# Optimization experiments

Measured on AMD Instinct MI355X. Metric: run time of the kernel, lower is better.

## Reference

```python
import jax, jax.numpy as jnp
import numpy as np

B, L, D_MODEL, H, DK = 4, 1024, 1024, 16, 64
FILTER_LENGTHS = (2, 4)
FMAX = max(FILTER_LENGTHS)


def setup_inputs() -> dict:
    key = jax.random.key(0)
    ks = jax.random.split(key, 12)
    s = 0.02
    inp = {
        "Q": jax.random.normal(ks[0], (B, L, D_MODEL), jnp.float32),
        "K": jax.random.normal(ks[1], (B, L, D_MODEL), jnp.float32),
        "V": jax.random.normal(ks[2], (B, L, D_MODEL), jnp.float32),
        "attn_mask": jnp.zeros((1,), jnp.bool_),
        "WQ": jax.random.normal(ks[3], (D_MODEL, H * DK), jnp.float32) * s,
        "bQ": jnp.zeros((H * DK,), jnp.float32),
        "WK": jax.random.normal(ks[4], (D_MODEL, H * DK), jnp.float32) * s,
        "bK": jnp.zeros((H * DK,), jnp.float32),
        "WV": jax.random.normal(ks[5], (D_MODEL, H * DK), jnp.float32) * s,
        "bV": jnp.zeros((H * DK,), jnp.float32),
        "Wfc": jax.random.normal(ks[6], (H * DK, D_MODEL), jnp.float32) * s,
        "bfc": jnp.zeros((D_MODEL,), jnp.float32),
        "conv_q": jax.random.normal(ks[7], (H * DK, H * DK, FMAX), jnp.float32) * s,
        "conv_k": jax.random.normal(ks[8], (H * DK, H * DK, FMAX), jnp.float32) * s,
        "w": jax.random.normal(ks[9], (len(FILTER_LENGTHS),), jnp.float32),
    }
    return inp


def _get_conv(x4, conv, w):
    # x4: (b, h, l, d_k) -> ACAT.get_conv with torch-identical raw reshapes
    b, h, l, d_k = x4.shape
    sig = x4.reshape(b, h * d_k, l)            # raw row-major reshape (as torch)
    pad = jnp.pad(sig, ((0, 0), (0, 0), (FMAX // 2, FMAX // 2)))
    idx = jnp.arange(l)[:, None] + jnp.arange(FMAX)[None, :]   # (l, FMAX) unfold windows
    seq = pad[:, :, idx]                        # (b, d, l, FMAX)
    f_s = jnp.array(FILTER_LENGTHS, dtype=sig.dtype)
    w_f = f_s * w                               # einsum('f,f->f')
    ind = jnp.argmax(w_f)
    flen = jnp.array(FILTER_LENGTHS)[ind]
    mask = (jnp.arange(FMAX) < flen).astype(sig.dtype)
    seq = seq * mask                            # zero out trailing taps
    out = jnp.einsum('bdlf,dof->blo', seq, conv)  # o = h*d_k
    return out.reshape(b, h, l, d_k)            # raw reshape as in torch code


def reference(Q, K, V, attn_mask, WQ, bQ, WK, bK, WV, bV, Wfc, bfc, conv_q, conv_k, w):
    b, l, _ = Q.shape
    q = (Q @ WQ + bQ).reshape(b, l, H, DK).transpose(0, 2, 1, 3)  # (b,h,l,dk)
    k = (K @ WK + bK).reshape(b, l, H, DK).transpose(0, 2, 1, 3)
    v = (V @ WV + bV).reshape(b, l, H, DK).transpose(0, 2, 1, 3)
    q = _get_conv(q, conv_q, w) + q
    k = _get_conv(k, conv_k, w) + k
    scores = jnp.einsum('bhqd,bhkd->bhqk', q, k) / np.sqrt(DK).astype(np.float32)
    attn = jax.nn.softmax(scores, axis=-1)
    ctx = jnp.einsum('bhqk,bhkd->bhqd', attn, v)
    ctx = ctx.transpose(0, 2, 1, 3).reshape(b, l, H * DK)
    out = ctx @ Wfc + bfc
    return out
```

## Files before the change

### kernel.cpp

```cpp
#include <hip/hip_runtime.h>
#include <hip/hip_bf16.h>

typedef _Float16 f16;
typedef _Float16 f16x2 __attribute__((ext_vector_type(2)));
typedef _Float16 f16x4 __attribute__((ext_vector_type(4)));
typedef _Float16 f16x8 __attribute__((ext_vector_type(8)));
typedef float f32x4 __attribute__((ext_vector_type(4)));

__device__ __forceinline__ f16x2 pkrtz(float a, float b) {
    auto r = __builtin_amdgcn_cvt_pkrtz(a, b);
    f16x2 o; o[0] = (f16)r[0]; o[1] = (f16)r[1];
    return o;
}

#define XT_ROWS 1027
#define XT_BSTRIDE (XT_ROWS * 1024)

__device__ __forceinline__ void gload16(const f16* g, f16* l) {
    __builtin_amdgcn_global_load_lds(
        (const __attribute__((address_space(1))) void*)g,
        (__attribute__((address_space(3))) void*)l, 16, 0, 0);
}

__device__ __forceinline__ void stage_tile(const f16* src, int ld, f16* lds)
{
    const int tid = threadIdx.x;
    const int w512 = (tid >> 6) << 9;
    #pragma unroll
    for (int q = 0; q < 4; ++q) {
        const int s = q * 256 + tid;
        const int row = s >> 3;
        const int col = ((s & 7) ^ (row & 7)) << 3;
        gload16(src + row * ld + col, lds + (q << 11) + w512);
    }
}

__device__ __forceinline__ void stage64(const f16* src, int ld, f16* lds)
{
    const int tid = threadIdx.x;
    const int w512 = (tid >> 6) << 9;
    #pragma unroll
    for (int q = 0; q < 2; ++q) {
        const int s = q * 256 + tid;
        const int row = s >> 3;
        const int col = ((s & 7) ^ (row & 7)) << 3;
        gload16(src + row * ld + col, lds + (q << 11) + w512);
    }
}

template <int CONV>
__device__ __forceinline__ void gemm_core64(
    const f16* __restrict__ A, int lda, int m0,
    const f16* __restrict__ Bt, int ldb, int K,
    f16* Alds, f16* Blds, f32x4 acc[4][4])
{
    const int tid = threadIdx.x;
    const int lid = tid & 63;
    const int wv  = tid >> 6;
    const int wm  = (wv >> 1) * 64;
    const int wn  = (wv & 1) * 64;
    const int g   = lid >> 4;
    const int r15 = lid & 15;

    stage_tile(A + m0 * lda, lda, Alds);
    stage_tile(Bt, ldb, Blds);
    asm volatile("s_waitcnt vmcnt(0)" ::: "memory");
    __builtin_amdgcn_s_barrier();

    for (int k0 = 0; k0 < K; k0 += 64) {
        f16x8 af[2][4], bf[2][4];
        #pragma unroll
        for (int kc = 0; kc < 2; ++kc) {
            #pragma unroll
            for (int mi = 0; mi < 4; ++mi) {
                const int row = wm + mi * 16 + r15;
                af[kc][mi] = *(const f16x8*)(Alds + row * 64 +
                                             (((kc * 4 + g) ^ (row & 7)) << 3));
            }
            #pragma unroll
            for (int nj = 0; nj < 4; ++nj) {
                const int row = wn + nj * 16 + r15;
                bf[kc][nj] = *(const f16x8*)(Blds + row * 64 +
                                             (((kc * 4 + g) ^ (row & 7)) << 3));
            }
        }
        asm volatile("s_waitcnt lgkmcnt(0)" ::: "memory");
        __builtin_amdgcn_sched_barrier(0);
        __builtin_amdgcn_s_barrier();
        const int k1 = k0 + 64;
        if (k1 < K) {
            const f16* Asrc;
            if (CONV) Asrc = A + (m0 + (k1 >> 10)) * lda + (k1 & 1023);
            else      Asrc = A + m0 * lda + k1;
            stage_tile(Asrc, lda, Alds);
            stage_tile(Bt + k1, ldb, Blds);
        }
        __builtin_amdgcn_sched_barrier(0);
        #pragma unroll
        for (int kc = 0; kc < 2; ++kc)
            #pragma unroll
            for (int mi = 0; mi < 4; ++mi)
                #pragma unroll
                for (int nj = 0; nj < 4; ++nj)
                    acc[mi][nj] = __builtin_amdgcn_mfma_f32_16x16x32_f16(
                        af[kc][mi], bf[kc][nj], acc[kc == 0 ? mi : mi][nj],
                        0, 0, 0),
                    acc[mi][nj] = acc[mi][nj];
        __builtin_amdgcn_sched_barrier(0);
        asm volatile("s_waitcnt vmcnt(0)" ::: "memory");
        __builtin_amdgcn_s_barrier();
    }
}

__global__ __launch_bounds__(256) void k_cvt_all(
    const float* __restrict__ Q, const float* __restrict__ K,
    const float* __restrict__ V, f16* __restrict__ Qh,
    f16* __restrict__ Kh, f16* __restrict__ Vh)
{
    const int bid = blockIdx.x;
    const int which = bid >> 12;
    const int i = (bid & 4095) * 256 + threadIdx.x;
    const float* in = which == 0 ? Q : which == 1 ? K : V;
    f16* out = which == 0 ? Qh : which == 1 ? Kh : Vh;
    float4 v = ((const float4*)in)[i];
    f16x4 o;
    o[0] = (f16)v.x; o[1] = (f16)v.y; o[2] = (f16)v.z; o[3] = (f16)v.w;
    ((f16x4*)out)[i] = o;
}

__global__ __launch_bounds__(256) void k_wtrans(
    const float* __restrict__ WQ, const float* __restrict__ WK,
    const float* __restrict__ WV, const float* __restrict__ Wfc,
    f16* __restrict__ WQt, f16* __restrict__ WKt,
    f16* __restrict__ WVt, f16* __restrict__ WFt)
{
    const int z = blockIdx.z;
    const float* in = z == 0 ? WQ : z == 1 ? WK : z == 2 ? WV : Wfc;
    f16* out = z == 0 ? WQt : z == 1 ? WKt : z == 2 ? WVt : WFt;
    __shared__ float tile[32][33];
    int c0 = blockIdx.x * 32, r0 = blockIdx.y * 32;
    int tx = threadIdx.x, ty = threadIdx.y;
    #pragma unroll
    for (int i = ty; i < 32; i += 8)
        tile[i][tx] = in[(size_t)(r0 + i) * 1024 + c0 + tx];
    __syncthreads();
    #pragma unroll
    for (int i = ty; i < 32; i += 8)
        out[(size_t)(c0 + i) * 1024 + r0 + tx] = (f16)tile[tx][i];
}

__global__ __launch_bounds__(256) void k_ctrans(
    const float* __restrict__ convq, const float* __restrict__ convk,
    f16* __restrict__ CTq, f16* __restrict__ CTk)
{
    const float* in = blockIdx.z ? convk : convq;
    f16* out = blockIdx.z ? CTk : CTq;
    __shared__ float tile[32][33];
    int c0 = blockIdx.x * 32, r0 = blockIdx.y * 32;
    int tx = threadIdx.x, ty = threadIdx.y;
    #pragma unroll
    for (int i = ty; i < 32; i += 8)
        tile[i][tx] = in[(size_t)(r0 + i) * 4096 + c0 + tx];
    __syncthreads();
    #pragma unroll
    for (int i = ty; i < 32; i += 8)
        out[(size_t)(c0 + i) * 1024 + r0 + tx] = (f16)tile[tx][i];
}

__global__ __launch_bounds__(256) void k_transpose_pad(
    const f16* __restrict__ qx4, const f16* __restrict__ kx4,
    f16* __restrict__ XtQ, f16* __restrict__ XtK)
{
    int z = blockIdx.z, b = z & 3, ten = z >> 2;
    const f16* in = (ten ? kx4 : qx4) + (size_t)b * 1048576;
    f16* out = (ten ? XtK : XtQ) + (size_t)b * XT_BSTRIDE;
    __shared__ f16 tile[32][33];
    int c0 = blockIdx.x * 32;
    int tp0 = blockIdx.y * 32;
    int tx = threadIdx.x, ty = threadIdx.y;
    #pragma unroll
    for (int i = ty; i < 32; i += 8) {
        int t = tp0 + tx - 2;
        tile[i][tx] = (t >= 0 && t < 1024) ? in[(c0 + i) * 1024 + t] : (f16)0.f;
    }
    __syncthreads();
    #pragma unroll
    for (int i = ty; i < 32; i += 8) {
        int tp = tp0 + i;
        if (tp < XT_ROWS) out[tp * 1024 + c0 + tx] = tile[tx][i];
    }
}

__global__ __launch_bounds__(256) void k_gemm_proj(
    const f16* __restrict__ Qh, const f16* __restrict__ Kh, const f16* __restrict__ Vh,
    const f16* __restrict__ WQt, const f16* __restrict__ WKt, const f16* __restrict__ WVt,
    const float* __restrict__ bQ, const float* __restrict__ bK, const float* __restrict__ bV,
    f16* __restrict__ qx4, f16* __restrict__ kx4, f16* __restrict__ vT)
{
    __shared__ __align__(16) f16 smem[16384];
    const int nid = blockIdx.x + blockIdx.y * 8 + blockIdx.z * 256;
    const int wgid = (nid & 7) * 96 + (nid >> 3);
    const int xw = wgid & 7, yw = (wgid >> 3) & 31, z = wgid >> 8;
    const f16* A  = z == 0 ? Qh : z == 1 ? Kh : Vh;
    const f16* Bt = z == 0 ? WQt : z == 1 ? WKt : WVt;
    const float* bias = z == 0 ? bQ : z == 1 ? bK : bV;
    f16* dst = z == 0 ? qx4 : z == 1 ? kx4 : vT;
    const int m0 = yw * 128, n0 = xw * 128;
    f32x4 acc[4][4] = {};
    gemm_core64<0>(A, 1024, m0, Bt + n0 * 1024, 1024, 1024,
                   smem, smem + 8192, acc);

    const int tid = threadIdx.x, lid = tid & 63, wv = tid >> 6;
    const int wm = (wv >> 1) * 64, g = lid >> 4, r15 = lid & 15;
    f16* T = smem;
    #pragma unroll
    for (int p = 0; p < 2; ++p) {
        __syncthreads();
        if ((wv & 1) == p) {
            #pragma unroll
            for (int nj = 0; nj < 4; ++nj) {
                const int col = n0 + p * 64 + nj * 16 + r15;
                const float bv = bias[col];
                #pragma unroll
                for (int mi = 0; mi < 4; ++mi)
                    #pragma unroll
                    for (int j = 0; j < 4; ++j)
                        T[(wm + mi * 16 + g * 4 + j) * 72 + nj * 16 + r15] =
                            (f16)(acc[mi][nj][j] + bv);
            }
        }
        __syncthreads();
        if (z != 2) {
            const int h = (n0 + p * 64) >> 6;
            #pragma unroll
            for (int q = 0; q < 4; ++q) {
                const int cid = q * 256 + tid;
                const int row = cid >> 3, c = (cid & 7) * 8;
                f16x8 v = *(const f16x8*)(T + row * 72 + c);
                const int grow = m0 + row;
                const int b = grow >> 10, l = grow & 1023;
                *(f16x8*)(dst + b * 1048576 + h * 65536 + l * 64 + c) = v;
            }
        } else {
            const int h = (n0 + p * 64) >> 6;
            #pragma unroll
            for (int q = 0; q < 4; ++q) {
                const int cid = q * 256 + tid;
                const int d = cid >> 4, lc = (cid & 15) * 8;
                f16x8 v;
                #pragma unroll
                for (int e = 0; e < 8; ++e) v[e] = T[(lc + e) * 72 + d];
                const int grow = m0 + lc;
                const int b = grow >> 10, l = grow & 1023;
                *(f16x8*)(dst + b * 1048576 + h * 65536 + d * 1024 + l) = v;
            }
        }
    }
}

__global__ __launch_bounds__(256) void k_gemm_conv(
    const f16* __restrict__ XtQ, const f16* __restrict__ XtK,
    const f16* __restrict__ CTq, const f16* __restrict__ CTk,
    f16* __restrict__ qx4, f16* __restrict__ kx4,
    const float* __restrict__ wvec)
{
    __shared__ __align__(16) f16 smem[16384];
    const int nid = blockIdx.x + blockIdx.y * 8 + blockIdx.z * 64;
    const int z = nid & 7;
    const int inner = nid >> 3;
    const int yw = inner & 7;
    const int xw = inner >> 3;
    const int b = z & 3, ten = z >> 2;
    const f16* Xt = (ten ? XtK : XtQ) + (size_t)b * XT_BSTRIDE;
    const f16* CT = ten ? CTk : CTq;
    f16* dst = (ten ? kx4 : qx4) + (size_t)b * 1048576;

    const int flen = (2.f * wvec[0] >= 4.f * wvec[1]) ? 2 : 4;
    const int K = flen << 10;

    const int m0 = yw * 128, n0 = xw * 128;
    f32x4 acc[4][4] = {};
    gemm_core64<1>(Xt, 1024, m0, CT + n0 * 4096, 4096, K,
                   smem, smem + 8192, acc);

    const int tid = threadIdx.x, lid = tid & 63, wv = tid >> 6;
    const int wm = (wv >> 1) * 64, g = lid >> 4, r15 = lid & 15;
    f16* T = smem;
    #pragma unroll
    for (int p = 0; p < 2; ++p) {
        __syncthreads();
        if ((wv & 1) == p) {
            #pragma unroll
            for (int nj = 0; nj < 4; ++nj)
                #pragma unroll
                for (int mi = 0; mi < 4; ++mi)
                    #pragma unroll
                    for (int j = 0; j < 4; ++j)
                        T[(wm + mi * 16 + g * 4 + j) * 72 + nj * 16 + r15] =
                            (f16)acc[mi][nj][j];
        }
        __syncthreads();
        #pragma unroll
        for (int q = 0; q < 4; ++q) {
            const int cid = q * 256 + tid;
            const int row = cid >> 3, c = (cid & 7) * 8;
            f16x8 v = *(const f16x8*)(T + row * 72 + c);
            f16* pdst = dst + (size_t)(m0 + row) * 1024 + n0 + p * 64 + c;
            f16x8 r = *(const f16x8*)pdst;
            f16x8 o2;
            #pragma unroll
            for (int e = 0; e < 8; ++e)
                o2[e] = (f16)((float)v[e] + (float)r[e]);
            *(f16x8*)pdst = o2;
        }
    }
}

__device__ __forceinline__ void attn_tile(
    const f16* KL, const f16* VL,
    const f16* Kn, const f16* Vn, f16* KLn, f16* VLn, bool doStage,
    const f16x8 qf[2][2], f32x4 o[2][4], f32x4 lsum[2], int g, int r15)
{
    f16x8 kf[4][2];
    #pragma unroll
    for (int nj = 0; nj < 4; ++nj)
        #pragma unroll
        for (int kc = 0; kc < 2; ++kc) {
            const int row = nj * 16 + r15;
            kf[nj][kc] = *(const f16x8*)(KL + row * 64 +
                                         (((kc * 4 + g) ^ (row & 7)) << 3));
        }
    f16x4 vlo[4][2], vhi[4][2];
    #pragma unroll
    for (int db = 0; db < 4; ++db)
        #pragma unroll
        for (int ch = 0; ch < 2; ++ch) {
            const int row = db * 16 + r15;
            const int c1 = ch * 4 + (g >> 1);
            const int c2 = c1 + 2;
            const int sub = (g & 1) * 4;
            vlo[db][ch] = *(const f16x4*)(VL + row * 64 +
                                          ((c1 ^ (row & 7)) << 3) + sub);
            vhi[db][ch] = *(const f16x4*)(VL + row * 64 +
                                          ((c2 ^ (row & 7)) << 3) + sub);
        }
    asm volatile("s_waitcnt lgkmcnt(0)" ::: "memory");
    __builtin_amdgcn_sched_barrier(0);
    __builtin_amdgcn_s_barrier();
    if (doStage) {
        stage64(Kn, 64, KLn);
        stage64(Vn, 1024, VLn);
    }
    __builtin_amdgcn_sched_barrier(0);
    f32x4 sacc[2][4] = {};
    #pragma unroll
    for (int nj = 0; nj < 4; ++nj)
        #pragma unroll
        for (int kc = 0; kc < 2; ++kc) {
            sacc[0][nj] = __builtin_amdgcn_mfma_f32_16x16x32_f16(
                kf[nj][kc], qf[0][kc], sacc[0][nj], 0, 0, 0);
            sacc[1][nj] = __builtin_amdgcn_mfma_f32_16x16x32_f16(
                kf[nj][kc], qf[1][kc], sacc[1][nj], 0, 0, 0);
        }
    #pragma unroll
    for (int qh = 0; qh < 2; ++qh) {
        f32x4 pe[4];
        #pragma unroll
        for (int nj = 0; nj < 4; ++nj) {
            #pragma unroll
            for (int j = 0; j < 4; ++j)
                pe[nj][j] = __expf(sacc[qh][nj][j] - 2.0f);
            lsum[qh] += pe[nj];
        }
        f16x8 pb[2];
        #pragma unroll
        for (int ch = 0; ch < 2; ++ch) {
            union { f16x2 h2[4]; f16x8 v8; } u;
            u.h2[0] = pkrtz(pe[2 * ch][0], pe[2 * ch][1]);
            u.h2[1] = pkrtz(pe[2 * ch][2], pe[2 * ch][3]);
            u.h2[2] = pkrtz(pe[2 * ch + 1][0], pe[2 * ch + 1][1]);
            u.h2[3] = pkrtz(pe[2 * ch + 1][2], pe[2 * ch + 1][3]);
            pb[ch] = u.v8;
        }
        #pragma unroll
        for (int db = 0; db < 4; ++db)
            #pragma unroll
            for (int ch = 0; ch < 2; ++ch) {
                union { f16x4 h4[2]; f16x8 v8; } w;
                w.h4[0] = vlo[db][ch];
                w.h4[1] = vhi[db][ch];
                o[qh][db] = __builtin_amdgcn_mfma_f32_16x16x32_f16(
                    w.v8, pb[ch], o[qh][db], 0, 0, 0);
            }
    }
    __builtin_amdgcn_sched_barrier(0);
    asm volatile("s_waitcnt vmcnt(0)" ::: "memory");
    __builtin_amdgcn_s_barrier();
}

__global__ __launch_bounds__(256) void k_attn(
    const f16* __restrict__ qn, const f16* __restrict__ kn,
    const f16* __restrict__ vT, f16* __restrict__ ctx)
{
    __shared__ __align__(16) f16 lds[4][4096];
    const int bh = blockIdx.x, b = bh >> 4, h = bh & 15;
    const f16* Qp = qn + (size_t)b * 1048576 + h * 65536;
    const f16* Kp = kn + (size_t)b * 1048576 + h * 65536;
    const f16* Vp = vT + (size_t)b * 1048576 + h * 65536;
    const int tid = threadIdx.x, lid = tid & 63, wv = tid >> 6;
    const int g = lid >> 4, r15 = lid & 15;
    const int q0 = blockIdx.y * 128 + wv * 32;

    f16x8 qf[2][2];
    #pragma unroll
    for (int qh = 0; qh < 2; ++qh)
        #pragma unroll
        for (int kc = 0; kc < 2; ++kc) {
            f16x8 t = *(const f16x8*)(Qp + (q0 + qh * 16 + r15) * 64 + kc * 32 + g * 8);
            #pragma unroll
            for (int e = 0; e < 8; ++e) t[e] = t[e] * (f16)0.125f;
            qf[qh][kc] = t;
        }

    f32x4 o[2][4] = {};
    f32x4 lsum[2] = {};

    stage64(Kp, 64, lds[0]);
    stage64(Vp, 1024, lds[1]);
    asm volatile("s_waitcnt vmcnt(0)" ::: "memory");
    __builtin_amdgcn_s_barrier();

    for (int tt = 0; tt < 8; ++tt) {
        const int t1 = 2 * tt + 1;
        attn_tile(lds[0], lds[1], Kp + t1 * 4096, Vp + t1 * 64,
                  lds[2], lds[3], true, qf, o, lsum, g, r15);
        attn_tile(lds[2], lds[3], Kp + (t1 + 1) * 4096, Vp + (t1 + 1) * 64,
                  lds[0], lds[1], tt < 7, qf, o, lsum, g, r15);
    }

    float inv[2];
    #pragma unroll
    for (int qh = 0; qh < 2; ++qh) {
        float lr = lsum[qh][0] + lsum[qh][1] + lsum[qh][2] + lsum[qh][3];
        lr += __shfl_xor(lr, 16);
        lr += __shfl_xor(lr, 32);
        inv[qh] = 1.0f / lr;
    }
    f16* Olds = &lds[0][0] + wv * (32 * 72);
    #pragma unroll
    for (int qh = 0; qh < 2; ++qh)
        #pragma unroll
        for (int db = 0; db < 4; ++db) {
            const int row = qh * 16 + r15, col = db * 16 + g * 4;
            *(f16x2*)(Olds + row * 72 + col) =
                pkrtz(o[qh][db][0] * inv[qh], o[qh][db][1] * inv[qh]);
            *(f16x2*)(Olds + row * 72 + col + 2) =
                pkrtz(o[qh][db][2] * inv[qh], o[qh][db][3] * inv[qh]);
        }
    asm volatile("s_waitcnt lgkmcnt(0)" ::: "memory");
    __builtin_amdgcn_sched_barrier(0);
    #pragma unroll
    for (int p = 0; p < 4; ++p) {
        const int row = p * 8 + (lid >> 3);
        const int c8 = (lid & 7) * 8;
        f16x8 v = *(const f16x8*)(Olds + row * 72 + c8);
        *(f16x8*)(ctx + (size_t)b * 1048576 + (q0 + row) * 1024 + h * 64 + c8) = v;
    }
}

__global__ __launch_bounds__(256) void k_gemm_final(
    const f16* __restrict__ ctx, const f16* __restrict__ WFt,
    const float* __restrict__ bfc, float* __restrict__ out)
{
    __shared__ __align__(16) f16 smem[16384];
    const int nid = blockIdx.x + blockIdx.y * 8;
    const int wgid = (nid & 7) * 32 + (nid >> 3);
    const int xw = wgid & 7, yw = wgid >> 3;
    const int m0 = yw * 128, n0 = xw * 128;
    f32x4 acc[4][4] = {};
    gemm_core64<0>(ctx, 1024, m0, WFt + n0 * 1024, 1024, 1024,
                   smem, smem + 8192, acc);

    const int tid = threadIdx.x, lid = tid & 63, wv = tid >> 6;
    const int wm = (wv >> 1) * 64, wn = (wv & 1) * 64, g = lid >> 4, r15 = lid & 15;
    #pragma unroll
    for (int nj = 0; nj < 4; ++nj) {
        const int col = n0 + wn + nj * 16 + r15;
        const float bv = bfc[col];
        #pragma unroll
        for (int mi = 0; mi < 4; ++mi)
            #pragma unroll
            for (int j = 0; j < 4; ++j) {
                const int row = m0 + wm + mi * 16 + g * 4 + j;
                out[(size_t)row * 1024 + col] = acc[mi][nj][j] + bv;
            }
    }
}

extern "C" void kernel_launch(void* const* d_in, const int* in_sizes, int n_in,
                              void* d_out, int out_size, void* d_ws, size_t ws_size,
                              hipStream_t stream)
{
    (void)in_sizes; (void)n_in; (void)out_size; (void)ws_size;
    const float* Q     = (const float*)d_in[0];
    const float* K     = (const float*)d_in[1];
    const float* V     = (const float*)d_in[2];
    const float* WQ    = (const float*)d_in[4];
    const float* bQ    = (const float*)d_in[5];
    const float* WK    = (const float*)d_in[6];
    const float* bK    = (const float*)d_in[7];
    const float* WV    = (const float*)d_in[8];
    const float* bV    = (const float*)d_in[9];
    const float* Wfc   = (const float*)d_in[10];
    const float* bfc   = (const float*)d_in[11];
    const float* convq = (const float*)d_in[12];
    const float* convk = (const float*)d_in[13];
    const float* w     = (const float*)d_in[14];

    char* ws = (char*)d_ws;
    f16* qx4   = (f16*)(ws + 0);
    f16* kx4   = (f16*)(ws + 8388608);
    f16* vT    = (f16*)(ws + 16777216);
    f16* WFt   = (f16*)(ws + 25165824);
    f16* Qh    = (f16*)(ws + 27262976);
    f16* Kh    = (f16*)(ws + 35651584);
    f16* Vh    = (f16*)(ws + 44040192);
    f16* WQt   = (f16*)(ws + 52428800);
    f16* WKt   = (f16*)(ws + 54525952);
    f16* WVt   = (f16*)(ws + 56623104);
    f16* CTq   = (f16*)(ws + 58720256);
    f16* XtQ   = (f16*)(ws + 27262976);
    f16* XtK   = (f16*)(ws + 35676160);
    f16* CTk   = (f16*)(ws + 44089344);
    f16* ctxb  = (f16*)(ws + 27262976);

    dim3 b256(256), bT(32, 8);

    k_cvt_all<<<12288, b256, 0, stream>>>(Q, K, V, Qh, Kh, Vh);
    k_wtrans<<<dim3(32, 32, 4), bT, 0, stream>>>(WQ, WK, WV, Wfc,
                                                 WQt, WKt, WVt, WFt);
    k_gemm_proj<<<dim3(8, 32, 3), b256, 0, stream>>>(Qh, Kh, Vh, WQt, WKt, WVt,
                                                     bQ, bK, bV, qx4, kx4, vT);
    k_transpose_pad<<<dim3(32, 33, 8), bT, 0, stream>>>(qx4, kx4, XtQ, XtK);
    k_ctrans<<<dim3(128, 32, 2), bT, 0, stream>>>(convq, convk, CTq, CTk);
    k_gemm_conv<<<dim3(8, 8, 8), b256, 0, stream>>>(XtQ, XtK, CTq, CTk,
                                                    qx4, kx4, w);
    k_attn<<<dim3(64, 8), b256, 0, stream>>>(qx4, kx4, vT, ctxb);
    k_gemm_final<<<dim3(8, 32), b256, 0, stream>>>(ctxb, WFt, bfc, (float*)d_out);
}
```

Before: 174.3 us.

## Fuse fp32-to-fp16 input conversion into projection GEMM A-tile loading

```diff
diff --git a/kernel.cpp b/kernel.cpp
--- a/kernel.cpp
+++ b/kernel.cpp
@@ -45,6 +45,37 @@
         const int row = s >> 3;
         const int col = ((s & 7) ^ (row & 7)) << 3;
         gload16(src + row * ld + col, lds + (q << 11) + w512);
+    }
+}
+
+__device__ __forceinline__ void a32_load(const float* src, int lda,
+                                         float4 lo[4], float4 hi[4])
+{
+    const int tid = threadIdx.x;
+    #pragma unroll
+    for (int q = 0; q < 4; ++q) {
+        const int s = q * 256 + tid;
+        const int row = s >> 3;
+        const int col = ((s & 7) ^ (row & 7)) << 3;
+        const float* p = src + (size_t)row * lda + col;
+        lo[q] = *(const float4*)p;
+        hi[q] = *(const float4*)(p + 4);
+    }
+}
+
+__device__ __forceinline__ void a32_write(const float4 lo[4], const float4 hi[4],
+                                          f16* lds)
+{
+    const int tid = threadIdx.x;
+    #pragma unroll
+    for (int q = 0; q < 4; ++q) {
+        const int s = q * 256 + tid;
+        f16x8 v;
+        v[0] = (f16)lo[q].x; v[1] = (f16)lo[q].y;
+        v[2] = (f16)lo[q].z; v[3] = (f16)lo[q].w;
+        v[4] = (f16)hi[q].x; v[5] = (f16)hi[q].y;
+        v[6] = (f16)hi[q].z; v[7] = (f16)hi[q].w;
+        *(f16x8*)(lds + (s << 3)) = v;
     }
 }
 
@@ -103,29 +134,73 @@
                 #pragma unroll
                 for (int nj = 0; nj < 4; ++nj)
                     acc[mi][nj] = __builtin_amdgcn_mfma_f32_16x16x32_f16(
-                        af[kc][mi], bf[kc][nj], acc[kc == 0 ? mi : mi][nj],
-                        0, 0, 0),
-                    acc[mi][nj] = acc[mi][nj];
+                        af[kc][mi], bf[kc][nj], acc[mi][nj], 0, 0, 0);
         __builtin_amdgcn_sched_barrier(0);
         asm volatile("s_waitcnt vmcnt(0)" ::: "memory");
         __builtin_amdgcn_s_barrier();
     }
 }
 
-__global__ __launch_bounds__(256) void k_cvt_all(
-    const float* __restrict__ Q, const float* __restrict__ K,
-    const float* __restrict__ V, f16* __restrict__ Qh,
-    f16* __restrict__ Kh, f16* __restrict__ Vh)
-{
-    const int bid = blockIdx.x;
-    const int which = bid >> 12;
-    const int i = (bid & 4095) * 256 + threadIdx.x;
-    const float* in = which == 0 ? Q : which == 1 ? K : V;
-    f16* out = which == 0 ? Qh : which == 1 ? Kh : Vh;
-    float4 v = ((const float4*)in)[i];
-    f16x4 o;
-    o[0] = (f16)v.x; o[1] = (f16)v.y; o[2] = (f16)v.z; o[3] = (f16)v.w;
-    ((f16x4*)out)[i] = o;
+__device__ __forceinline__ void gemm_core_a32(
+    const float* __restrict__ A, int lda, int m0,
+    const f16* __restrict__ Bt, int ldb, int K,
+    f16* Alds, f16* Blds, f32x4 acc[4][4])
+{
+    const int tid = threadIdx.x;
+    const int lid = tid & 63;
+    const int wv  = tid >> 6;
+    const int wm  = (wv >> 1) * 64;
+    const int wn  = (wv & 1) * 64;
+    const int g   = lid >> 4;
+    const int r15 = lid & 15;
+
+    float4 lo[4], hi[4];
+    a32_load(A + (size_t)m0 * lda, lda, lo, hi);
+    stage_tile(Bt, ldb, Blds);
+    a32_write(lo, hi, Alds);
+    asm volatile("s_waitcnt vmcnt(0) lgkmcnt(0)" ::: "memory");
+    __builtin_amdgcn_s_barrier();
+
+    for (int k0 = 0; k0 < K; k0 += 64) {
+        const int k1 = k0 + 64;
+        const bool nxt = k1 < K;
+        if (nxt) a32_load(A + (size_t)m0 * lda + k1, lda, lo, hi);
+        f16x8 af[2][4], bf[2][4];
+        #pragma unroll
+        for (int kc = 0; kc < 2; ++kc) {
+            #pragma unroll
+            for (int mi = 0; mi < 4; ++mi) {
+                const int row = wm + mi * 16 + r15;
+                af[kc][mi] = *(const f16x8*)(Alds + row * 64 +
+                                             (((kc * 4 + g) ^ (row & 7)) << 3));
+            }
+            #pragma unroll
+            for (int nj = 0; nj < 4; ++nj) {
+                const int row = wn + nj * 16 + r15;
+                bf[kc][nj] = *(const f16x8*)(Blds + row * 64 +
+                                             (((kc * 4 + g) ^ (row & 7)) << 3));
+            }
+        }
+        asm volatile("s_waitcnt lgkmcnt(0)" ::: "memory");
+        __builtin_amdgcn_sched_barrier(0);
+        __builtin_amdgcn_s_barrier();
+        if (nxt) stage_tile(Bt + k1, ldb, Blds);
+        __builtin_amdgcn_sched_barrier(0);
+        #pragma unroll
+        for (int kc = 0; kc < 2; ++kc)
+            #pragma unroll
+            for (int mi = 0; mi < 4; ++mi)
+                #pragma unroll
+                for (int nj = 0; nj < 4; ++nj)
+                    acc[mi][nj] = __builtin_amdgcn_mfma_f32_16x16x32_f16(
+                        af[kc][mi], bf[kc][nj], acc[mi][nj], 0, 0, 0);
+        __builtin_amdgcn_sched_barrier(0);
+        if (nxt) {
+            a32_write(lo, hi, Alds);
+            asm volatile("s_waitcnt vmcnt(0) lgkmcnt(0)" ::: "memory");
+            __builtin_amdgcn_s_barrier();
+        }
+    }
 }
 
 __global__ __launch_bounds__(256) void k_wtrans(
@@ -192,7 +267,8 @@
 }
 
 __global__ __launch_bounds__(256) void k_gemm_proj(
-    const f16* __restrict__ Qh, const f16* __restrict__ Kh, const f16* __restrict__ Vh,
+    const float* __restrict__ Q, const float* __restrict__ K,
+    const float* __restrict__ V,
     const f16* __restrict__ WQt, const f16* __restrict__ WKt, const f16* __restrict__ WVt,
     const float* __restrict__ bQ, const float* __restrict__ bK, const float* __restrict__ bV,
     f16* __restrict__ qx4, f16* __restrict__ kx4, f16* __restrict__ vT)
@@ -201,14 +277,14 @@
     const int nid = blockIdx.x + blockIdx.y * 8 + blockIdx.z * 256;
     const int wgid = (nid & 7) * 96 + (nid >> 3);
     const int xw = wgid & 7, yw = (wgid >> 3) & 31, z = wgid >> 8;
-    const f16* A  = z == 0 ? Qh : z == 1 ? Kh : Vh;
+    const float* A = z == 0 ? Q : z == 1 ? K : V;
     const f16* Bt = z == 0 ? WQt : z == 1 ? WKt : WVt;
     const float* bias = z == 0 ? bQ : z == 1 ? bK : bV;
     f16* dst = z == 0 ? qx4 : z == 1 ? kx4 : vT;
     const int m0 = yw * 128, n0 = xw * 128;
     f32x4 acc[4][4] = {};
-    gemm_core64<0>(A, 1024, m0, Bt + n0 * 1024, 1024, 1024,
-                   smem, smem + 8192, acc);
+    gemm_core_a32(A, 1024, m0, Bt + n0 * 1024, 1024, 1024,
+                  smem, smem + 8192, acc);
 
     const int tid = threadIdx.x, lid = tid & 63, wv = tid >> 6;
     const int wm = (wv >> 1) * 64, g = lid >> 4, r15 = lid & 15;
@@ -522,9 +598,6 @@
     f16* kx4   = (f16*)(ws + 8388608);
     f16* vT    = (f16*)(ws + 16777216);
     f16* WFt   = (f16*)(ws + 25165824);
-    f16* Qh    = (f16*)(ws + 27262976);
-    f16* Kh    = (f16*)(ws + 35651584);
-    f16* Vh    = (f16*)(ws + 44040192);
     f16* WQt   = (f16*)(ws + 52428800);
     f16* WKt   = (f16*)(ws + 54525952);
     f16* WVt   = (f16*)(ws + 56623104);
@@ -536,10 +609,9 @@
 
     dim3 b256(256), bT(32, 8);
 
-    k_cvt_all<<<12288, b256, 0, stream>>>(Q, K, V, Qh, Kh, Vh);
     k_wtrans<<<dim3(32, 32, 4), bT, 0, stream>>>(WQ, WK, WV, Wfc,
                                                  WQt, WKt, WVt, WFt);
-    k_gemm_proj<<<dim3(8, 32, 3), b256, 0, stream>>>(Qh, Kh, Vh, WQt, WKt, WVt,
+    k_gemm_proj<<<dim3(8, 32, 3), b256, 0, stream>>>(Q, K, V, WQt, WKt, WVt,
                                                      bQ, bK, bV, qx4, kx4, vT);
     k_transpose_pad<<<dim3(32, 33, 8), bT, 0, stream>>>(qx4, kx4, XtQ, XtK);
     k_ctrans<<<dim3(128, 32, 2), bT, 0, stream>>>(convq, convk, CTq, CTk);
```

Result: slower. 193.3 us (+10.9%).
